# Kernel optimization log

Hardware: AMD Instinct MI355X
Metric: run time of the kernel (lower is better)

The kernel has to match this reference:

```python
import jax, jax.numpy as jnp
import numpy as np

B, N, C, H, NRES = 32, 1024, 384, 1024, 20
NTAB = 21  # 20 aa + unknown, per AlphaFold residue_constants


def setup_inputs() -> dict:
    key = jax.random.key(0)
    ks = jax.random.split(key, 16)
    s = 0.02
    inp = {}
    inp['act'] = jax.random.normal(ks[0], (B, N, C), jnp.float32)
    inp['angles'] = jax.random.normal(ks[1], (B, N, 7, 2), jnp.float32)
    inp['rigids'] = jax.random.normal(ks[2], (B, N, 7), jnp.float32)
    inp['fixed_mask'] = jax.random.randint(ks[3], (B, N), 0, 2, jnp.int32)
    inp['seq_t'] = jax.random.randint(ks[4], (B, N), 0, NRES, jnp.int32)
    inp['residx_atom37_to_atom14'] = jax.random.randint(ks[5], (B, N, 37), 0, 14, jnp.int32)
    inp['ln_g'] = jnp.ones((C,), jnp.float32)
    inp['ln_b'] = jnp.zeros((C,), jnp.float32)
    inp['w1'] = jax.random.normal(ks[6], (C, H), jnp.float32) * s
    inp['b1'] = jnp.zeros((H,), jnp.float32)
    inp['w2'] = jax.random.normal(ks[7], (H, H), jnp.float32) * s
    inp['b2'] = jnp.zeros((H,), jnp.float32)
    inp['w3'] = jax.random.normal(ks[8], (H, NRES), jnp.float32) * s
    inp['b3'] = jnp.zeros((NRES,), jnp.float32)
    # stand-in residue_constants tables (same shapes/dtypes as AlphaFold's)
    inp['default_frames'] = jax.random.normal(ks[9], (NTAB, 8, 4, 4), jnp.float32)
    inp['group_idx'] = jax.random.randint(ks[10], (NTAB, 14), 0, 8, jnp.int32)
    inp['atom14_mask'] = (jax.random.uniform(ks[11], (NTAB, 14)) > 0.3).astype(jnp.float32)
    inp['atom37_mask'] = (jax.random.uniform(ks[12], (NTAB, 37)) > 0.3).astype(jnp.float32)
    inp['lit_positions'] = jax.random.normal(ks[13], (NTAB, 14, 3), jnp.float32)
    return inp


def quat_to_rot(q):
    q = q / jnp.sqrt(jnp.sum(q * q, axis=-1, keepdims=True) + 1e-8)
    w, x, y, z = q[..., 0], q[..., 1], q[..., 2], q[..., 3]
    r = jnp.stack([
        1 - 2 * (y * y + z * z), 2 * (x * y - w * z), 2 * (x * z + w * y),
        2 * (x * y + w * z), 1 - 2 * (x * x + z * z), 2 * (y * z - w * x),
        2 * (x * z - w * y), 2 * (y * z + w * x), 1 - 2 * (x * x + y * y)
    ], axis=-1)
    return r.reshape(q.shape[:-1] + (3, 3))


def compose(r1, t1, r2, t2):
    # rigid composition: (r1, t1) o (r2, t2)
    return (jnp.einsum('...ij,...jk->...ik', r1, r2),
            jnp.einsum('...ij,...j->...i', r1, t2) + t1)


def reference(act, angles, rigids, fixed_mask, seq_t, residx_atom37_to_atom14,
              ln_g, ln_b, w1, b1, w2, b2, w3, b3,
              default_frames, group_idx, atom14_mask, atom37_mask, lit_positions):
    # --- small MLP head ---
    mu = jnp.mean(act, axis=-1, keepdims=True)
    var = jnp.var(act, axis=-1, keepdims=True)
    h = (act - mu) / jnp.sqrt(var + 1e-5) * ln_g + ln_b
    h = jax.nn.relu(h @ w1 + b1)
    h = jax.nn.relu(h @ w2 + b2)
    logits = h @ w3 + b3                                # [B,N,20]
    p_0t = jax.nn.softmax(logits, axis=-1)
    seq0 = jnp.argmax(p_0t, axis=-1).astype(jnp.int32)
    seq0 = seq0 * (1 - fixed_mask) + seq_t * fixed_mask  # [B,N]

    # --- backbone frame from quaternion rigids ---
    rb = quat_to_rot(rigids[..., :4])                    # [B,N,3,3]
    tb = rigids[..., 4:]                                 # [B,N,3]

    # --- torsion_angles_to_frames ---
    df = default_frames[seq0]                            # [B,N,8,4,4]
    dr, dt = df[..., :3, :3], df[..., :3, 3]
    sin, cos = angles[..., 0], angles[..., 1]            # [B,N,7]
    z1 = jnp.zeros_like(sin[..., :1])
    sin8 = jnp.concatenate([z1, sin], axis=-1)           # backbone group has angle 0
    cos8 = jnp.concatenate([jnp.ones_like(z1), cos], axis=-1)
    zz, oo = jnp.zeros_like(sin8), jnp.ones_like(sin8)
    rx = jnp.stack([oo, zz, zz, zz, cos8, -sin8, zz, sin8, cos8], axis=-1)
    rx = rx.reshape(sin8.shape + (3, 3))                 # rotation about x-axis
    fr = jnp.einsum('bngij,bngjk->bngik', dr, rx)        # frames to backbone (pre-chain)
    ft = dt
    # chain chi2->chi1, chi3->chi2, chi4->chi3
    r5, t5 = compose(fr[..., 4, :, :], ft[..., 4, :], fr[..., 5, :, :], ft[..., 5, :])
    r6, t6 = compose(r5, t5, fr[..., 6, :, :], ft[..., 6, :])
    r7, t7 = compose(r6, t6, fr[..., 7, :, :], ft[..., 7, :])
    frot = jnp.concatenate([fr[..., :5, :, :], r5[..., None, :, :], r6[..., None, :, :], r7[..., None, :, :]], axis=-3)
    ftr = jnp.concatenate([ft[..., :5, :], t5[..., None, :], t6[..., None, :], t7[..., None, :]], axis=-2)
    grot, gtr = compose(rb[..., None, :, :], tb[..., None, :], frot, ftr)  # [B,N,8,3,3],[B,N,8,3]

    # --- frames_and_literature_positions_to_atom14_pos ---
    gi = group_idx[seq0]                                 # [B,N,14]
    ar = jnp.take_along_axis(grot, jnp.broadcast_to(gi[..., None, None], gi.shape + (3, 3)), axis=2)
    at = jnp.take_along_axis(gtr, jnp.broadcast_to(gi[..., None], gi.shape + (3,)), axis=2)
    lit = lit_positions[seq0]                            # [B,N,14,3]
    m14 = atom14_mask[seq0]                              # [B,N,14]
    pred = (jnp.einsum('bnaij,bnaj->bnai', ar, lit) + at) * m14[..., None]

    # --- atom14 -> atom37 gather ---
    idx = residx_atom37_to_atom14
    final = jnp.take_along_axis(pred, jnp.broadcast_to(idx[..., None], idx.shape + (3,)), axis=2)
    m37 = atom37_mask[seq0]                              # [B,N,37]
    return logits, seq0, pred, final, m14, m37
```

## Files before the change

### kernel.cpp

```cpp
#include <hip/hip_runtime.h>
#include <math.h>

#define B_ 32
#define N_ 1024
#define C_ 384
#define H_ 1024
#define NRES 20
#define NTAB 21
#define M_TOTAL (B_*N_)
#define BK 32

typedef __attribute__((ext_vector_type(8))) short bf16x8;
typedef __attribute__((ext_vector_type(4))) float f32x4;

#define GLOAD_LDS(gptr, lptr) \
    __builtin_amdgcn_global_load_lds( \
        (const __attribute__((address_space(1))) void*)(gptr), \
        (__attribute__((address_space(3))) void*)(lptr), 16, 0, 0)

__device__ inline short bf16_rne(float v) {
    unsigned u = __float_as_uint(v);
    unsigned r = u + 0x7fffu + ((u >> 16) & 1u);
    return (short)(r >> 16);
}
__device__ inline void split2(float v, short& h, short& l) {
    unsigned u = __float_as_uint(v);
    unsigned r = (u + 0x7fffu + ((u >> 16) & 1u)) & 0xffff0000u;
    h = (short)(r >> 16);
    l = bf16_rne(v - __uint_as_float(r));
}

__global__ __launch_bounds__(256) void ln_split_kernel(const float* __restrict__ act,
                                                       const float* __restrict__ lng,
                                                       const float* __restrict__ lnb,
                                                       short* __restrict__ Xh,
                                                       short* __restrict__ Xl) {
    int wave = threadIdx.x >> 6;
    int lane = threadIdx.x & 63;
    int row  = blockIdx.x * 4 + wave;
    const float* x = act + (size_t)row * C_;
    float v[6];
    float s = 0.f;
#pragma unroll
    for (int i = 0; i < 6; i++) { v[i] = x[lane + i*64]; s += v[i]; }
#pragma unroll
    for (int off = 32; off > 0; off >>= 1) s += __shfl_xor(s, off, 64);
    float mu = s * (1.0f/384.0f);
    float vs = 0.f;
#pragma unroll
    for (int i = 0; i < 6; i++) { float d = v[i]-mu; vs += d*d; }
#pragma unroll
    for (int off = 32; off > 0; off >>= 1) vs += __shfl_xor(vs, off, 64);
    float rstd = 1.0f / sqrtf(vs * (1.0f/384.0f) + 1e-5f);
#pragma unroll
    for (int i = 0; i < 6; i++) {
        int col = lane + i*64;
        float y = (v[i] - mu) * rstd * lng[col] + lnb[col];
        short h, l; split2(y, h, l);
        Xh[(size_t)row * C_ + col] = h;
        Xl[(size_t)row * C_ + col] = l;
    }
}

__global__ __launch_bounds__(256) void conv_w_kernel(const float* __restrict__ w,
                                                     short* __restrict__ th,
                                                     short* __restrict__ tl,
                                                     int K, int N, int Npad) {
    __shared__ float t[32][33];
    int n0 = blockIdx.x * 32, k0 = blockIdx.y * 32;
    int tx = threadIdx.x & 31, ty = threadIdx.x >> 5;
#pragma unroll
    for (int i = ty; i < 32; i += 8) {
        int k = k0 + i, n = n0 + tx;
        t[i][tx] = (n < N) ? w[(size_t)k * N + n] : 0.f;
    }
    __syncthreads();
#pragma unroll
    for (int i = ty; i < 32; i += 8) {
        int n = n0 + i, k = k0 + tx;
        short h, l; split2(t[tx][i], h, l);
        th[(size_t)n * K + k] = h;
        tl[(size_t)n * K + k] = l;
    }
}

template<bool FUSE>
__global__ __launch_bounds__(512, 2) void presplit_gemm256(
    const short* __restrict__ Ahg, const short* __restrict__ Alg,
    const short* __restrict__ BTh, const short* __restrict__ BTl,
    const float* __restrict__ bias,
    short* __restrict__ Ch, short* __restrict__ Cl,
    int K, int ldc,
    const short* __restrict__ W3h, const short* __restrict__ W3l,
    float* __restrict__ logit_acc, int m0c)
{
    __shared__ short P[4][2][256][32];
    const int BUFS = 256*32;
    int tid = threadIdx.x;
    int m0 = blockIdx.x * 256;
    int n0 = blockIdx.y * 256;
    int lane = tid & 63, wv = tid >> 6;
    int wr = wv >> 2, wc = wv & 3;
    int fm = lane & 15, kg = lane >> 4;

    int pl = wv >> 1, hf = wv & 1;
    const short* gsrc = (pl == 0) ? Ahg : (pl == 1) ? Alg : (pl == 2) ? BTh : BTl;
    int base = (pl < 2) ? m0 : n0;
    int swcb = (lane & 3) ^ ((lane >> 3) & 3);
    const short* gp = gsrc + (size_t)(base + hf*128 + (lane >> 2)) * K + swcb * 8;
    short* lpl = &P[pl][0][0][0] + hf * (128*32);

    int sz = (kg ^ ((fm >> 1) & 3)) * 8;
    const short* raH = &P[0][0][wr*128 + fm][0] + sz;
    const short* raL = &P[1][0][wr*128 + fm][0] + sz;
    const short* rbH = &P[2][0][wc*64  + fm][0] + sz;
    const short* rbL = &P[3][0][wc*64  + fm][0] + sz;

#define STAGE(c, bsel, koff) \
    GLOAD_LDS(gp + (size_t)((c)*16) * K + (koff), lpl + (bsel)*BUFS + (c)*512)

#define TRIPLE(ai, aj, AH, AL, BH, BL) { \
    f32x4 cc = acc[ai][aj]; \
    cc = __builtin_amdgcn_mfma_f32_16x16x32_bf16(AL, BH, cc, 0, 0, 0); \
    cc = __builtin_amdgcn_mfma_f32_16x16x32_bf16(AH, BL, cc, 0, 0, 0); \
    cc = __builtin_amdgcn_mfma_f32_16x16x32_bf16(AH, BH, cc, 0, 0, 0); \
    acc[ai][aj] = cc; }

    f32x4 acc[8][4] = {};
    const int NT = K / BK;

#pragma unroll
    for (int c = 0; c < 8; c++) STAGE(c, 0, 0);

    for (int t = 0; t < NT; ++t) {
        int cur = t & 1, nxt = cur ^ 1;
        size_t koff = (size_t)(t + 1) * BK;
        bool pf = (t + 1 < NT);

        bf16x8 a_h[4], a_l[4], b_h[4], b_l[4];

        if (pf) {
            STAGE(0, nxt, koff); STAGE(1, nxt, koff);
            asm volatile("s_waitcnt vmcnt(2)" ::: "memory");
        } else {
            asm volatile("s_waitcnt vmcnt(0)" ::: "memory");
        }
        __builtin_amdgcn_s_barrier();
        __builtin_amdgcn_sched_barrier(0);
#pragma unroll
        for (int i = 0; i < 4; i++) {
            a_h[i] = *(const bf16x8*)(raH + cur*BUFS + i*512);
            a_l[i] = *(const bf16x8*)(raL + cur*BUFS + i*512);
        }
#pragma unroll
        for (int j = 0; j < 2; j++) {
            b_h[j] = *(const bf16x8*)(rbH + cur*BUFS + j*512);
            b_l[j] = *(const bf16x8*)(rbL + cur*BUFS + j*512);
        }
        __builtin_amdgcn_s_setprio(1);
#pragma unroll
        for (int i = 0; i < 4; i++)
#pragma unroll
            for (int j = 0; j < 2; j++) TRIPLE(i, j, a_h[i], a_l[i], b_h[j], b_l[j]);
        __builtin_amdgcn_s_setprio(0);
        __builtin_amdgcn_s_barrier();

        if (pf) { STAGE(2, nxt, koff); STAGE(3, nxt, koff); }
#pragma unroll
        for (int j = 0; j < 2; j++) {
            b_h[2+j] = *(const bf16x8*)(rbH + cur*BUFS + (2+j)*512);
            b_l[2+j] = *(const bf16x8*)(rbL + cur*BUFS + (2+j)*512);
        }
        __builtin_amdgcn_s_barrier();
        __builtin_amdgcn_s_setprio(1);
#pragma unroll
        for (int i = 0; i < 4; i++)
#pragma unroll
            for (int j = 0; j < 2; j++) TRIPLE(i, 2+j, a_h[i], a_l[i], b_h[2+j], b_l[2+j]);
        __builtin_amdgcn_s_setprio(0);
        __builtin_amdgcn_s_barrier();

        if (pf) { STAGE(4, nxt, koff); STAGE(5, nxt, koff); }
#pragma unroll
        for (int i = 0; i < 4; i++) {
            a_h[i] = *(const bf16x8*)(raH + cur*BUFS + (4+i)*512);
            a_l[i] = *(const bf16x8*)(raL + cur*BUFS + (4+i)*512);
        }
        __builtin_amdgcn_s_barrier();
        __builtin_amdgcn_s_setprio(1);
#pragma unroll
        for (int i = 0; i < 4; i++)
#pragma unroll
            for (int j = 0; j < 2; j++) TRIPLE(4+i, j, a_h[i], a_l[i], b_h[j], b_l[j]);
        __builtin_amdgcn_s_setprio(0);
        __builtin_amdgcn_s_barrier();

        if (pf) { STAGE(6, nxt, koff); STAGE(7, nxt, koff); }
        __builtin_amdgcn_s_barrier();
        __builtin_amdgcn_s_setprio(1);
#pragma unroll
        for (int i = 0; i < 4; i++)
#pragma unroll
            for (int j = 0; j < 2; j++) TRIPLE(4+i, 2+j, a_h[i], a_l[i], b_h[2+j], b_l[2+j]);
        __builtin_amdgcn_s_setprio(0);
        __builtin_amdgcn_s_barrier();
    }

    if (!FUSE) {
#pragma unroll
        for (int i = 0; i < 8; i++)
#pragma unroll
            for (int j = 0; j < 4; j++) {
                int col = n0 + wc*64 + j*16 + fm;
                float bs = bias[col];
#pragma unroll
                for (int r2 = 0; r2 < 4; r2++) {
                    int row = m0 + wr*128 + i*16 + kg*4 + r2;
                    float v = fmaxf(acc[i][j][r2] + bs, 0.f);
                    short h, l; split2(v, h, l);
                    Ch[(size_t)row * ldc + col] = h;
                    Cl[(size_t)row * ldc + col] = l;
                }
            }
    } else {
        unsigned* L32 = (unsigned*)&P[0][0][0][0];
#pragma unroll
        for (int h = 0; h < 2; h++) {
            if (wr == h) {
#pragma unroll
                for (int i = 0; i < 8; i++)
#pragma unroll
                    for (int j = 0; j < 4; j++) {
                        int col = wc*64 + j*16 + fm;
                        float bs = bias[n0 + col];
#pragma unroll
                        for (int r2 = 0; r2 < 4; r2++) {
                            int lr = i*16 + kg*4 + r2;
                            float v = fmaxf(acc[i][j][r2] + bs, 0.f);
                            short sh, sl; split2(v, sh, sl);
                            L32[lr*256 + (col ^ ((lr & 15) << 1))] =
                                ((unsigned)(unsigned short)sh << 16) | (unsigned short)sl;
                        }
                    }
            }
            __syncthreads();
            f32x4 pl0 = {}, pl1 = {};
            int rbase = (wv*16 + fm) * 256;
            int swr = fm << 1;
#pragma unroll
            for (int s = 0; s < 8; s++) {
                int kb = s*32 + kg*8;
                bf16x8 A_h, A_l;
#pragma unroll
                for (int c = 0; c < 8; c++) {
                    unsigned u = L32[rbase + ((kb + c) ^ swr)];
                    A_h[c] = (short)(u >> 16);
                    A_l[c] = (short)(u & 0xffffu);
                }
                size_t wk = (size_t)(n0 + kb);
                bf16x8 B0h = *(const bf16x8*)&W3h[(size_t)fm * H_ + wk];
                bf16x8 B0l = *(const bf16x8*)&W3l[(size_t)fm * H_ + wk];
                bf16x8 B1h = *(const bf16x8*)&W3h[(size_t)(16 + fm) * H_ + wk];
                bf16x8 B1l = *(const bf16x8*)&W3l[(size_t)(16 + fm) * H_ + wk];
                pl0 = __builtin_amdgcn_mfma_f32_16x16x32_bf16(A_l, B0h, pl0, 0, 0, 0);
                pl0 = __builtin_amdgcn_mfma_f32_16x16x32_bf16(A_h, B0l, pl0, 0, 0, 0);
                pl0 = __builtin_amdgcn_mfma_f32_16x16x32_bf16(A_h, B0h, pl0, 0, 0, 0);
                pl1 = __builtin_amdgcn_mfma_f32_16x16x32_bf16(A_l, B1h, pl1, 0, 0, 0);
                pl1 = __builtin_amdgcn_mfma_f32_16x16x32_bf16(A_h, B1l, pl1, 0, 0, 0);
                pl1 = __builtin_amdgcn_mfma_f32_16x16x32_bf16(A_h, B1h, pl1, 0, 0, 0);
            }
            int growb = m0c + m0 + h*128 + wv*16 + kg*4;
#pragma unroll
            for (int r2 = 0; r2 < 4; r2++)
                atomicAdd(&logit_acc[(size_t)(growb + r2) * NRES + fm], pl0[r2]);
            if (fm < 4) {
#pragma unroll
                for (int r2 = 0; r2 < 4; r2++)
                    atomicAdd(&logit_acc[(size_t)(growb + r2) * NRES + 16 + fm], pl1[r2]);
            }
            __syncthreads();
        }
    }
#undef STAGE
#undef TRIPLE
}

__global__ __launch_bounds__(256) void argmax_kernel(
    float* __restrict__ logits, const float* __restrict__ b3,
    const int* __restrict__ fixed_mask, const int* __restrict__ seq_t,
    float* __restrict__ seq_out, int* __restrict__ seq_int, int m0c)
{
    int grow = m0c + blockIdx.x * 256 + threadIdx.x;
    float* lg = logits + (size_t)grow * NRES;
    float best = -1e30f; int bi = 0;
#pragma unroll
    for (int n = 0; n < NRES; n++) {
        float s = lg[n] + b3[n];
        lg[n] = s;
        if (s > best) { best = s; bi = n; }
    }
    int fmk = fixed_mask[grow];
    int sv = fmk ? seq_t[grow] : bi;
    seq_int[grow] = sv;
    seq_out[grow] = (float)sv;
}

__global__ __launch_bounds__(128) void geom_kernel(
    const float* __restrict__ angles, const float* __restrict__ rigids,
    const int* __restrict__ seq0i, const int* __restrict__ residx,
    const float* __restrict__ dframes, const int* __restrict__ gidx,
    const float* __restrict__ a14m, const float* __restrict__ a37m,
    const float* __restrict__ litp,
    float* __restrict__ out_pred, float* __restrict__ out_final,
    float* __restrict__ out_m14, float* __restrict__ out_m37)
{
    __shared__ float sdf[NTAB*8*16];
    __shared__ int   sgi[NTAB*14];
    __shared__ float sm14[NTAB*14];
    __shared__ float sm37[NTAB*37];
    __shared__ float slit[NTAB*14*3];
    __shared__ float predL[128][43];

    for (int i = threadIdx.x; i < NTAB*128; i += 128) sdf[i] = dframes[i];
    for (int i = threadIdx.x; i < NTAB*14; i += 128) { sgi[i] = gidx[i]; sm14[i] = a14m[i]; }
    for (int i = threadIdx.x; i < NTAB*37; i += 128) sm37[i] = a37m[i];
    for (int i = threadIdx.x; i < NTAB*42; i += 128) slit[i] = litp[i];
    __syncthreads();

    int p = blockIdx.x * 128 + threadIdx.x;
    int s = seq0i[p];

    const float* rg = rigids + (size_t)p * 7;
    float qw = rg[0], qx = rg[1], qy = rg[2], qz = rg[3];
    float tbx = rg[4], tby = rg[5], tbz = rg[6];
    float qn = 1.0f / sqrtf(qw*qw + qx*qx + qy*qy + qz*qz + 1e-8f);
    qw *= qn; qx *= qn; qy *= qn; qz *= qn;
    float rb[9];
    rb[0] = 1.f - 2.f*(qy*qy + qz*qz); rb[1] = 2.f*(qx*qy - qw*qz); rb[2] = 2.f*(qx*qz + qw*qy);
    rb[3] = 2.f*(qx*qy + qw*qz); rb[4] = 1.f - 2.f*(qx*qx + qz*qz); rb[5] = 2.f*(qy*qz - qw*qx);
    rb[6] = 2.f*(qx*qz - qw*qy); rb[7] = 2.f*(qy*qz + qw*qx); rb[8] = 1.f - 2.f*(qx*qx + qy*qy);

    float fr[8][9], ft[8][3];
    const float* ang = angles + (size_t)p * 14;
#pragma unroll
    for (int g = 0; g < 8; g++) {
        const float* df = &sdf[(s*8 + g)*16];
        float c, sn;
        if (g == 0) { c = 1.f; sn = 0.f; }
        else { sn = ang[(g-1)*2 + 0]; c = ang[(g-1)*2 + 1]; }
#pragma unroll
        for (int i = 0; i < 3; i++) {
            float d0 = df[i*4+0], d1 = df[i*4+1], d2 = df[i*4+2];
            fr[g][i*3+0] = d0;
            fr[g][i*3+1] = d1*c + d2*sn;
            fr[g][i*3+2] = d2*c - d1*sn;
            ft[g][i] = df[i*4+3];
        }
    }
#pragma unroll
    for (int g = 5; g <= 7; g++) {
        float r[9], t[3];
        const float* r1 = fr[g-1];
        const float* t1 = ft[g-1];
#pragma unroll
        for (int i = 0; i < 3; i++) {
#pragma unroll
            for (int j = 0; j < 3; j++)
                r[i*3+j] = r1[i*3+0]*fr[g][0*3+j] + r1[i*3+1]*fr[g][1*3+j] + r1[i*3+2]*fr[g][2*3+j];
            t[i] = r1[i*3+0]*ft[g][0] + r1[i*3+1]*ft[g][1] + r1[i*3+2]*ft[g][2] + t1[i];
        }
#pragma unroll
        for (int i = 0; i < 9; i++) fr[g][i] = r[i];
#pragma unroll
        for (int i = 0; i < 3; i++) ft[g][i] = t[i];
    }
#pragma unroll
    for (int g = 0; g < 8; g++) {
        float r[9], t[3];
#pragma unroll
        for (int i = 0; i < 3; i++) {
#pragma unroll
            for (int j = 0; j < 3; j++)
                r[i*3+j] = rb[i*3+0]*fr[g][0*3+j] + rb[i*3+1]*fr[g][1*3+j] + rb[i*3+2]*fr[g][2*3+j];
            t[i] = rb[i*3+0]*ft[g][0] + rb[i*3+1]*ft[g][1] + rb[i*3+2]*ft[g][2];
        }
#pragma unroll
        for (int i = 0; i < 9; i++) fr[g][i] = r[i];
        ft[g][0]=t[0]+tbx; ft[g][1]=t[1]+tby; ft[g][2]=t[2]+tbz;
    }
#pragma unroll
    for (int g = 0; g < 8; g++) {
#pragma unroll
        for (int a = 0; a < 14; a++) {
            if (sgi[s*14 + a] == g) {
                float m  = sm14[s*14 + a];
                float lx = slit[(s*14 + a)*3 + 0];
                float ly = slit[(s*14 + a)*3 + 1];
                float lz = slit[(s*14 + a)*3 + 2];
                float px = (fr[g][0]*lx + fr[g][1]*ly + fr[g][2]*lz + ft[g][0]) * m;
                float py = (fr[g][3]*lx + fr[g][4]*ly + fr[g][5]*lz + ft[g][1]) * m;
                float pz = (fr[g][6]*lx + fr[g][7]*ly + fr[g][8]*lz + ft[g][2]) * m;
                predL[threadIdx.x][a*3+0] = px;
                predL[threadIdx.x][a*3+1] = py;
                predL[threadIdx.x][a*3+2] = pz;
                out_pred[((size_t)p*14 + a)*3 + 0] = px;
                out_pred[((size_t)p*14 + a)*3 + 1] = py;
                out_pred[((size_t)p*14 + a)*3 + 2] = pz;
            }
        }
    }
#pragma unroll
    for (int a = 0; a < 14; a++) out_m14[(size_t)p*14 + a] = sm14[s*14 + a];

    const int* idx = residx + (size_t)p * 37;
#pragma unroll
    for (int a = 0; a < 37; a++) {
        int id = idx[a];
        out_final[((size_t)p*37 + a)*3 + 0] = predL[threadIdx.x][id*3+0];
        out_final[((size_t)p*37 + a)*3 + 1] = predL[threadIdx.x][id*3+1];
        out_final[((size_t)p*37 + a)*3 + 2] = predL[threadIdx.x][id*3+2];
        out_m37[(size_t)p*37 + a] = sm37[s*37 + a];
    }
}

extern "C" void kernel_launch(void* const* d_in, const int* in_sizes, int n_in,
                              void* d_out, int out_size, void* d_ws, size_t ws_size,
                              hipStream_t stream) {
    const float* act        = (const float*)d_in[0];
    const float* angles     = (const float*)d_in[1];
    const float* rigids     = (const float*)d_in[2];
    const int*   fixed_mask = (const int*)d_in[3];
    const int*   seq_t      = (const int*)d_in[4];
    const int*   residx     = (const int*)d_in[5];
    const float* lng        = (const float*)d_in[6];
    const float* lnb        = (const float*)d_in[7];
    const float* w1         = (const float*)d_in[8];
    const float* b1         = (const float*)d_in[9];
    const float* w2         = (const float*)d_in[10];
    const float* b2         = (const float*)d_in[11];
    const float* w3         = (const float*)d_in[12];
    const float* b3         = (const float*)d_in[13];
    const float* dfr        = (const float*)d_in[14];
    const int*   gidx       = (const int*)d_in[15];
    const float* a14m       = (const float*)d_in[16];
    const float* a37m       = (const float*)d_in[17];
    const float* litp       = (const float*)d_in[18];

    float* out        = (float*)d_out;
    float* out_logits = out;
    float* out_seq    = out_logits + (size_t)M_TOTAL * NRES;
    float* out_pred   = out_seq    + (size_t)M_TOTAL;
    float* out_final  = out_pred   + (size_t)M_TOTAL * 42;
    float* out_m14    = out_final  + (size_t)M_TOTAL * 111;
    float* out_m37    = out_m14    + (size_t)M_TOTAL * 14;

    char* wsp = (char*)d_ws;
    int*   seq0i = (int*)wsp;   wsp += (size_t)M_TOTAL * sizeof(int);
    short* w1h   = (short*)wsp; wsp += (size_t)H_ * C_ * sizeof(short);
    short* w1l   = (short*)wsp; wsp += (size_t)H_ * C_ * sizeof(short);
    short* w2h   = (short*)wsp; wsp += (size_t)H_ * H_ * sizeof(short);
    short* w2l   = (short*)wsp; wsp += (size_t)H_ * H_ * sizeof(short);
    short* w3h   = (short*)wsp; wsp += (size_t)128 * H_ * sizeof(short);
    short* w3l   = (short*)wsp; wsp += (size_t)128 * H_ * sizeof(short);
    short* Xh    = (short*)wsp; wsp += (size_t)M_TOTAL * C_ * sizeof(short);
    short* Xl    = (short*)wsp; wsp += (size_t)M_TOTAL * C_ * sizeof(short);

    size_t fixed_bytes = (size_t)(wsp - (char*)d_ws);
    size_t per_row = 2ull * H_ * sizeof(short);
    size_t avail = ws_size - fixed_bytes;
    int chunkM = 4096;
    if (avail >= (size_t)M_TOTAL * per_row)      chunkM = M_TOTAL;
    else if (avail >= 16384ull * per_row)        chunkM = 16384;
    else if (avail >= 8192ull * per_row)         chunkM = 8192;

    short* H1h = (short*)wsp; wsp += (size_t)chunkM * H_ * sizeof(short);
    short* H1l = (short*)wsp;

    hipMemsetAsync(out_logits, 0, (size_t)M_TOTAL * NRES * sizeof(float), stream);

    conv_w_kernel<<<dim3(H_/32, C_/32), 256, 0, stream>>>(w1, w1h, w1l, C_, H_, H_);
    conv_w_kernel<<<dim3(H_/32, H_/32), 256, 0, stream>>>(w2, w2h, w2l, H_, H_, H_);
    conv_w_kernel<<<dim3(128/32, H_/32), 256, 0, stream>>>(w3, w3h, w3l, H_, NRES, 128);

    ln_split_kernel<<<M_TOTAL/4, 256, 0, stream>>>(act, lng, lnb, Xh, Xl);

    for (int c = 0; c < M_TOTAL / chunkM; c++) {
        int m0 = c * chunkM;
        presplit_gemm256<false><<<dim3(chunkM/256, H_/256), 512, 0, stream>>>(
            Xh + (size_t)m0 * C_, Xl + (size_t)m0 * C_, w1h, w1l, b1,
            H1h, H1l, C_, H_, nullptr, nullptr, nullptr, 0);
        presplit_gemm256<true><<<dim3(chunkM/256, H_/256), 512, 0, stream>>>(
            H1h, H1l, w2h, w2l, b2,
            nullptr, nullptr, H_, 0, w3h, w3l, out_logits, m0);
        argmax_kernel<<<chunkM/256, 256, 0, stream>>>(
            out_logits, b3, fixed_mask, seq_t, out_seq, seq0i, m0);
    }

    geom_kernel<<<M_TOTAL/128, 128, 0, stream>>>(angles, rigids, seq0i, residx,
                                                 dfr, gidx, a14m, a37m, litp,
                                                 out_pred, out_final, out_m14, out_m37);
}
```

Measured before the change: 467.9 us.

## Split geometry kernel into per-atom compute and per-atom37 gather kernels

Replaces the per-residue geometry kernel with two kernels. The first assigns one thread per atom14 and builds only that atom's frame, recomputing the chi chain as needed. The second assigns one thread per atom37 and gathers from the written pred buffer. This is meant to raise parallelism and coalescing of the strided per-residue stores, at the cost of redundant frame math, an extra launch, and re-reading pred from global memory.

Result: no change. 460.1 us (-1.7%).

```diff
diff --git a/kernel.cpp b/kernel.cpp
--- a/kernel.cpp
+++ b/kernel.cpp
@@ -305,29 +305,24 @@
     seq_out[grow] = (float)sv;
 }
 
-__global__ __launch_bounds__(128) void geom_kernel(
+__global__ __launch_bounds__(256) void geom_atom_kernel(
     const float* __restrict__ angles, const float* __restrict__ rigids,
-    const int* __restrict__ seq0i, const int* __restrict__ residx,
+    const int* __restrict__ seq0i,
     const float* __restrict__ dframes, const int* __restrict__ gidx,
-    const float* __restrict__ a14m, const float* __restrict__ a37m,
-    const float* __restrict__ litp,
-    float* __restrict__ out_pred, float* __restrict__ out_final,
-    float* __restrict__ out_m14, float* __restrict__ out_m37)
+    const float* __restrict__ a14m, const float* __restrict__ litp,
+    float* __restrict__ out_pred, float* __restrict__ out_m14)
 {
     __shared__ float sdf[NTAB*8*16];
     __shared__ int   sgi[NTAB*14];
     __shared__ float sm14[NTAB*14];
-    __shared__ float sm37[NTAB*37];
     __shared__ float slit[NTAB*14*3];
-    __shared__ float predL[128][43];
-
-    for (int i = threadIdx.x; i < NTAB*128; i += 128) sdf[i] = dframes[i];
-    for (int i = threadIdx.x; i < NTAB*14; i += 128) { sgi[i] = gidx[i]; sm14[i] = a14m[i]; }
-    for (int i = threadIdx.x; i < NTAB*37; i += 128) sm37[i] = a37m[i];
-    for (int i = threadIdx.x; i < NTAB*42; i += 128) slit[i] = litp[i];
+    for (int i = threadIdx.x; i < NTAB*128; i += 256) sdf[i] = dframes[i];
+    for (int i = threadIdx.x; i < NTAB*14; i += 256) { sgi[i] = gidx[i]; sm14[i] = a14m[i]; }
+    for (int i = threadIdx.x; i < NTAB*42; i += 256) slit[i] = litp[i];
     __syncthreads();
 
-    int p = blockIdx.x * 128 + threadIdx.x;
+    int idx = blockIdx.x * 256 + threadIdx.x;
+    int p = idx / 14, a = idx - p * 14;
     int s = seq0i[p];
 
     const float* rg = rigids + (size_t)p * 7;
@@ -340,87 +335,84 @@
     rb[3] = 2.f*(qx*qy + qw*qz); rb[4] = 1.f - 2.f*(qx*qx + qz*qz); rb[5] = 2.f*(qy*qz - qw*qx);
     rb[6] = 2.f*(qx*qz - qw*qy); rb[7] = 2.f*(qy*qz + qw*qx); rb[8] = 1.f - 2.f*(qx*qx + qy*qy);
 
-    float fr[8][9], ft[8][3];
     const float* ang = angles + (size_t)p * 14;
-#pragma unroll
-    for (int g = 0; g < 8; g++) {
-        const float* df = &sdf[(s*8 + g)*16];
+    int g = sgi[s*14 + a];
+
+    auto build = [&](int gg, float* r, float* t) {
+        const float* df = &sdf[(s*8 + gg)*16];
         float c, sn;
-        if (g == 0) { c = 1.f; sn = 0.f; }
-        else { sn = ang[(g-1)*2 + 0]; c = ang[(g-1)*2 + 1]; }
+        if (gg == 0) { c = 1.f; sn = 0.f; }
+        else { sn = ang[(gg-1)*2 + 0]; c = ang[(gg-1)*2 + 1]; }
 #pragma unroll
         for (int i = 0; i < 3; i++) {
             float d0 = df[i*4+0], d1 = df[i*4+1], d2 = df[i*4+2];
-            fr[g][i*3+0] = d0;
-            fr[g][i*3+1] = d1*c + d2*sn;
-            fr[g][i*3+2] = d2*c - d1*sn;
-            ft[g][i] = df[i*4+3];
-        }
-    }
-#pragma unroll
-    for (int g = 5; g <= 7; g++) {
-        float r[9], t[3];
-        const float* r1 = fr[g-1];
-        const float* t1 = ft[g-1];
-#pragma unroll
-        for (int i = 0; i < 3; i++) {
-#pragma unroll
-            for (int j = 0; j < 3; j++)
-                r[i*3+j] = r1[i*3+0]*fr[g][0*3+j] + r1[i*3+1]*fr[g][1*3+j] + r1[i*3+2]*fr[g][2*3+j];
-            t[i] = r1[i*3+0]*ft[g][0] + r1[i*3+1]*ft[g][1] + r1[i*3+2]*ft[g][2] + t1[i];
-        }
-#pragma unroll
-        for (int i = 0; i < 9; i++) fr[g][i] = r[i];
-#pragma unroll
-        for (int i = 0; i < 3; i++) ft[g][i] = t[i];
-    }
-#pragma unroll
-    for (int g = 0; g < 8; g++) {
-        float r[9], t[3];
-#pragma unroll
-        for (int i = 0; i < 3; i++) {
-#pragma unroll
-            for (int j = 0; j < 3; j++)
-                r[i*3+j] = rb[i*3+0]*fr[g][0*3+j] + rb[i*3+1]*fr[g][1*3+j] + rb[i*3+2]*fr[g][2*3+j];
-            t[i] = rb[i*3+0]*ft[g][0] + rb[i*3+1]*ft[g][1] + rb[i*3+2]*ft[g][2];
-        }
-#pragma unroll
-        for (int i = 0; i < 9; i++) fr[g][i] = r[i];
-        ft[g][0]=t[0]+tbx; ft[g][1]=t[1]+tby; ft[g][2]=t[2]+tbz;
-    }
-#pragma unroll
-    for (int g = 0; g < 8; g++) {
-#pragma unroll
-        for (int a = 0; a < 14; a++) {
-            if (sgi[s*14 + a] == g) {
-                float m  = sm14[s*14 + a];
-                float lx = slit[(s*14 + a)*3 + 0];
-                float ly = slit[(s*14 + a)*3 + 1];
-                float lz = slit[(s*14 + a)*3 + 2];
-                float px = (fr[g][0]*lx + fr[g][1]*ly + fr[g][2]*lz + ft[g][0]) * m;
-                float py = (fr[g][3]*lx + fr[g][4]*ly + fr[g][5]*lz + ft[g][1]) * m;
-                float pz = (fr[g][6]*lx + fr[g][7]*ly + fr[g][8]*lz + ft[g][2]) * m;
-                predL[threadIdx.x][a*3+0] = px;
-                predL[threadIdx.x][a*3+1] = py;
-                predL[threadIdx.x][a*3+2] = pz;
-                out_pred[((size_t)p*14 + a)*3 + 0] = px;
-                out_pred[((size_t)p*14 + a)*3 + 1] = py;
-                out_pred[((size_t)p*14 + a)*3 + 2] = pz;
+            r[i*3+0] = d0;
+            r[i*3+1] = d1*c + d2*sn;
+            r[i*3+2] = d2*c - d1*sn;
+            t[i] = df[i*4+3];
+        }
+    };
+
+    float R[9], T[3];
+    if (g < 5) {
+        build(g, R, T);
+    } else {
+        build(4, R, T);
+        for (int gg = 5; gg <= g; gg++) {
+            float f[9], tt[3], r2[9], t2[3];
+            build(gg, f, tt);
+#pragma unroll
+            for (int i = 0; i < 3; i++) {
+#pragma unroll
+                for (int j = 0; j < 3; j++)
+                    r2[i*3+j] = R[i*3+0]*f[0*3+j] + R[i*3+1]*f[1*3+j] + R[i*3+2]*f[2*3+j];
+                t2[i] = R[i*3+0]*tt[0] + R[i*3+1]*tt[1] + R[i*3+2]*tt[2] + T[i];
             }
-        }
-    }
-#pragma unroll
-    for (int a = 0; a < 14; a++) out_m14[(size_t)p*14 + a] = sm14[s*14 + a];
-
-    const int* idx = residx + (size_t)p * 37;
-#pragma unroll
-    for (int a = 0; a < 37; a++) {
-        int id = idx[a];
-        out_final[((size_t)p*37 + a)*3 + 0] = predL[threadIdx.x][id*3+0];
-        out_final[((size_t)p*37 + a)*3 + 1] = predL[threadIdx.x][id*3+1];
-        out_final[((size_t)p*37 + a)*3 + 2] = predL[threadIdx.x][id*3+2];
-        out_m37[(size_t)p*37 + a] = sm37[s*37 + a];
-    }
+#pragma unroll
+            for (int i = 0; i < 9; i++) R[i] = r2[i];
+#pragma unroll
+            for (int i = 0; i < 3; i++) T[i] = t2[i];
+        }
+    }
+
+    float Rg[9], Tg[3];
+#pragma unroll
+    for (int i = 0; i < 3; i++) {
+#pragma unroll
+        for (int j = 0; j < 3; j++)
+            Rg[i*3+j] = rb[i*3+0]*R[0*3+j] + rb[i*3+1]*R[1*3+j] + rb[i*3+2]*R[2*3+j];
+        Tg[i] = rb[i*3+0]*T[0] + rb[i*3+1]*T[1] + rb[i*3+2]*T[2];
+    }
+    Tg[0] += tbx; Tg[1] += tby; Tg[2] += tbz;
+
+    float m  = sm14[s*14 + a];
+    float lx = slit[(s*14 + a)*3 + 0];
+    float ly = slit[(s*14 + a)*3 + 1];
+    float lz = slit[(s*14 + a)*3 + 2];
+    out_pred[(size_t)idx*3 + 0] = (Rg[0]*lx + Rg[1]*ly + Rg[2]*lz + Tg[0]) * m;
+    out_pred[(size_t)idx*3 + 1] = (Rg[3]*lx + Rg[4]*ly + Rg[5]*lz + Tg[1]) * m;
+    out_pred[(size_t)idx*3 + 2] = (Rg[6]*lx + Rg[7]*ly + Rg[8]*lz + Tg[2]) * m;
+    out_m14[idx] = m;
+}
+
+__global__ __launch_bounds__(256) void final_gather_kernel(
+    const int* __restrict__ seq0i, const int* __restrict__ residx,
+    const float* __restrict__ a37m, const float* __restrict__ out_pred,
+    float* __restrict__ out_final, float* __restrict__ out_m37)
+{
+    __shared__ float sm37[NTAB*37];
+    for (int i = threadIdx.x; i < NTAB*37; i += 256) sm37[i] = a37m[i];
+    __syncthreads();
+
+    int idx = blockIdx.x * 256 + threadIdx.x;
+    int p = idx / 37, a = idx - p * 37;
+    int s = seq0i[p];
+    int id = residx[idx];
+    const float* src = out_pred + ((size_t)p*14 + id)*3;
+    out_final[(size_t)idx*3 + 0] = src[0];
+    out_final[(size_t)idx*3 + 1] = src[1];
+    out_final[(size_t)idx*3 + 2] = src[2];
+    out_m37[idx] = sm37[s*37 + a];
 }
 
 extern "C" void kernel_launch(void* const* d_in, const int* in_sizes, int n_in,
@@ -496,7 +488,8 @@
             out_logits, b3, fixed_mask, seq_t, out_seq, seq0i, m0);
     }
 
-    geom_kernel<<<M_TOTAL/128, 128, 0, stream>>>(angles, rigids, seq0i, residx,
-                                                 dfr, gidx, a14m, a37m, litp,
-                                                 out_pred, out_final, out_m14, out_m37);
-}
+    geom_atom_kernel<<<(M_TOTAL*14)/256, 256, 0, stream>>>(
+        angles, rigids, seq0i, dfr, gidx, a14m, litp, out_pred, out_m14);
+    final_gather_kernel<<<(M_TOTAL*37)/256, 256, 0, stream>>>(
+        seq0i, residx, a37m, out_pred, out_final, out_m37);
+}
```
